# Kernel optimization log

Hardware: AMD Instinct MI355X
Metric: run time of the kernel (lower is better)

The kernel has to match this reference:

```python
import jax, jax.numpy as jnp
import numpy as np

B_, H_, W_, C_ = 4, 128, 128, 256
HEADS = 8
SPLIT = (8, 32)
POS_DIM = ((C_ // 2) // 4) // 4  # DynamicPosBias(dim//4).pos_dim with dim=C//2 -> 8


def _rel_tables(Hsp, Wsp):
    # rpe_biases: all relative (dy, dx) offsets, shape [(2Hsp-1)*(2Wsp-1), 2]
    gy, gx = np.meshgrid(np.arange(1 - Hsp, Hsp), np.arange(1 - Wsp, Wsp), indexing='ij')
    biases = np.stack([gy.ravel(), gx.ravel()], axis=1).astype(np.float32)
    # relative_position_index: [N, N] lookup into the bias table
    ch, cw = np.meshgrid(np.arange(Hsp), np.arange(Wsp), indexing='ij')
    cf = np.stack([ch.ravel(), cw.ravel()])  # [2, N]
    rel = (cf[:, :, None] - cf[:, None, :]).transpose(1, 2, 0)
    rel[..., 0] += Hsp - 1
    rel[..., 1] += Wsp - 1
    rel[..., 0] *= 2 * Wsp - 1
    idx = rel.sum(-1)
    return jnp.asarray(biases), jnp.asarray(idx)


def _ln(x, g, b):
    m = x.mean(-1, keepdims=True)
    v = ((x - m) ** 2).mean(-1, keepdims=True)
    return (x - m) / jnp.sqrt(v + 1e-5) * g + b


def _dyn_pos(biases, pw, pb, g1, b1, w1, c1, g2, b2, w2, c2, g3, b3, w3, c3):
    # DynamicPosBias, residual=False: pos3(pos2(pos1(pos_proj(b))))
    p = biases @ pw + pb
    p = jax.nn.relu(_ln(p, g1, b1)) @ w1 + c1
    p = jax.nn.relu(_ln(p, g2, b2)) @ w2 + c2
    p = jax.nn.relu(_ln(p, g3, b3)) @ w3 + c3
    return p  # [num_rel, heads]


def _win_attn(q, k, v, Hsp, Wsp, H, W, heads, pos_table, rel_idx):
    B, L, Cb = q.shape
    N = Hsp * Wsp
    hd = Cb // heads
    scale = hd ** (-0.5)

    def part(t):  # (B, L, Cb) -> (B*nW, heads, N, hd)
        t = t.reshape(B, H // Hsp, Hsp, W // Wsp, Wsp, Cb)
        t = t.transpose(0, 1, 3, 2, 4, 5).reshape(-1, N, heads, hd)
        return t.transpose(0, 2, 1, 3)

    qw, kw, vw = part(q) * scale, part(k), part(v)
    attn = jnp.einsum('whnd,whmd->whnm', qw, kw)
    rpb = pos_table[rel_idx.reshape(-1)].reshape(N, N, heads).transpose(2, 0, 1)
    attn = jax.nn.softmax(attn + rpb[None], axis=-1)
    ow = jnp.einsum('whnm,whmd->whnd', attn, vw)
    ow = ow.transpose(0, 2, 1, 3).reshape(-1, N, Cb)
    # windows2img
    img = ow.reshape(B, H // Hsp, W // Wsp, Hsp, Wsp, Cb)
    img = img.transpose(0, 1, 3, 2, 4, 5).reshape(B, H * W, Cb)
    return img


def setup_inputs() -> dict:
    key = jax.random.key(0)
    ks = jax.random.split(key, 16)
    nrm = lambda k, shp: jax.random.normal(k, shp, jnp.float32) * 0.02
    P, hb = POS_DIM, HEADS // 2
    d = {}
    d['x'] = jax.random.normal(ks[0], (B_, H_ * W_, C_), jnp.float32)
    d['w_qkv'] = nrm(ks[1], (C_, 3 * C_))
    d['w_proj'] = nrm(ks[2], (C_, C_))
    d['b_proj'] = jnp.zeros((C_,), jnp.float32)
    d['w_dw'] = nrm(ks[3], (C_, 1, 3, 3))
    d['b_dw'] = jnp.zeros((C_,), jnp.float32)
    d['pp_w'] = nrm(ks[4], (2, 2, P))
    d['pp_b'] = jnp.zeros((2, P), jnp.float32)
    d['ln1_g'] = jnp.ones((2, P), jnp.float32)
    d['ln1_b'] = jnp.zeros((2, P), jnp.float32)
    d['l1_w'] = nrm(ks[5], (2, P, P))
    d['l1_b'] = jnp.zeros((2, P), jnp.float32)
    d['ln2_g'] = jnp.ones((2, P), jnp.float32)
    d['ln2_b'] = jnp.zeros((2, P), jnp.float32)
    d['l2_w'] = nrm(ks[6], (2, P, P))
    d['l2_b'] = jnp.zeros((2, P), jnp.float32)
    d['ln3_g'] = jnp.ones((2, P), jnp.float32)
    d['ln3_b'] = jnp.zeros((2, P), jnp.float32)
    d['l3_w'] = nrm(ks[7], (2, P, hb))
    d['l3_b'] = jnp.zeros((2, hb), jnp.float32)
    d['H'] = H_
    d['W'] = W_
    return d


def reference(x, w_qkv, w_proj, b_proj, w_dw, b_dw, pp_w, pp_b, ln1_g, ln1_b, l1_w, l1_b, ln2_g, ln2_b, l2_w, l2_b, ln3_g, ln3_b, l3_w, l3_b, H, W):
    B, L, C = x.shape
    Cb, hb = C // 2, HEADS // 2
    qkv = (x @ w_qkv).reshape(B, L, 3, C).transpose(2, 0, 1, 3)
    q, k, v = qkv[0], qkv[1], qkv[2]
    v_img = v.transpose(0, 2, 1).reshape(B, C, H, W)
    outs = []
    for br in range(2):  # two cross-shaped window branches (idx=0/1)
        Hsp, Wsp = SPLIT if br == 0 else (SPLIT[1], SPLIT[0])
        sl = slice(br * Cb, (br + 1) * Cb)
        biases, rel_idx = _rel_tables(Hsp, Wsp)
        pos = _dyn_pos(biases, pp_w[br], pp_b[br], ln1_g[br], ln1_b[br], l1_w[br], l1_b[br],
                       ln2_g[br], ln2_b[br], l2_w[br], l2_b[br], ln3_g[br], ln3_b[br], l3_w[br], l3_b[br])
        outs.append(_win_attn(q[..., sl], k[..., sl], v[..., sl], Hsp, Wsp, H, W, hb, pos, rel_idx))
    att = jnp.concatenate(outs, axis=-1)  # (B, L, C)
    # LePE: depthwise 3x3 conv on V (get_v, groups=dim)
    lepe = jax.lax.conv_general_dilated(v_img, w_dw, (1, 1), ((1, 1), (1, 1)),
                                        feature_group_count=C,
                                        dimension_numbers=('NCHW', 'OIHW', 'NCHW'))
    lepe = (lepe + b_dw[None, :, None, None]).transpose(0, 2, 3, 1).reshape(B, L, C)
    return (att + lepe) @ w_proj + b_proj
```

## Files before the change

### kernel.cpp

```cpp
#include <hip/hip_runtime.h>
#include <hip/hip_bf16.h>
#include <math.h>

#define B_ 4
#define HH 128
#define WW 128
#define CC 256
#define LL (HH * WW)
#define NROWS (B_ * LL)
#define NREL 945
#define SCALE 0.17677669529663687f
#define LOG2E 1.4426950408889634f
#define SCALE2 (0.17677669529663687f * 1.4426950408889634f)

typedef __attribute__((ext_vector_type(8))) _Float16 half8;
typedef __attribute__((ext_vector_type(2))) __fp16 fp16x2;
typedef __attribute__((ext_vector_type(4))) float f32x4;

__device__ __forceinline__ unsigned short f2h(float f) {
    union { _Float16 h; unsigned short u; } v;
    v.h = (_Float16)f;
    return v.u;
}
__device__ __forceinline__ float h2f(unsigned short u) {
    union { unsigned short u; _Float16 h; } v;
    v.u = u;
    return (float)v.h;
}
__device__ __forceinline__ float exp2_raw(float x) {
    float r;
    asm("v_exp_f32 %0, %1" : "=v"(r) : "v"(x));
    return r;
}
__device__ __forceinline__ void gl_lds16(const unsigned short* g, unsigned short* l) {
    __builtin_amdgcn_global_load_lds((const __attribute__((address_space(1))) void*)g,
                                     (__attribute__((address_space(3))) void*)l, 16, 0, 0);
}

__device__ inline void ln_relu8(float* v, const float* g, const float* b) {
    float m = 0.f;
#pragma unroll
    for (int j = 0; j < 8; j++) m += v[j];
    m *= 0.125f;
    float var = 0.f;
#pragma unroll
    for (int j = 0; j < 8; j++) { float d = v[j] - m; var += d * d; }
    var *= 0.125f;
    float inv = 1.0f / sqrtf(var + 1e-5f);
#pragma unroll
    for (int j = 0; j < 8; j++) {
        float xn = (v[j] - m) * inv * g[j] + b[j];
        v[j] = xn > 0.f ? xn : 0.f;
    }
}

__device__ inline void mat8x8(const float* in, float* out, const float* w, const float* bias) {
#pragma unroll
    for (int j = 0; j < 8; j++) {
        float s = bias[j];
#pragma unroll
        for (int i = 0; i < 8; i++) s = fmaf(in[i], w[i * 8 + j], s);
        out[j] = s;
    }
}

__global__ void pos_kernel(const float* __restrict__ pp_w, const float* __restrict__ pp_b,
                           const float* __restrict__ ln1_g, const float* __restrict__ ln1_b,
                           const float* __restrict__ l1_w, const float* __restrict__ l1_b,
                           const float* __restrict__ ln2_g, const float* __restrict__ ln2_b,
                           const float* __restrict__ l2_w, const float* __restrict__ l2_b,
                           const float* __restrict__ ln3_g, const float* __restrict__ ln3_b,
                           const float* __restrict__ l3_w, const float* __restrict__ l3_b,
                           float* __restrict__ pos) {
    const int br = blockIdx.x;
    const int Wsp = br ? 8 : 32;
    const int Hsp = br ? 32 : 8;
    const int W2 = 2 * Wsp - 1;
    const int nrel = (2 * Hsp - 1) * W2;
    for (int r = threadIdx.x; r < nrel; r += blockDim.x) {
        float dy = (float)(r / W2 - (Hsp - 1));
        float dx = (float)(r % W2 - (Wsp - 1));
        float p[8], t[8];
#pragma unroll
        for (int j = 0; j < 8; j++)
            p[j] = dy * pp_w[br * 16 + j] + dx * pp_w[br * 16 + 8 + j] + pp_b[br * 8 + j];
        ln_relu8(p, ln1_g + br * 8, ln1_b + br * 8);
        mat8x8(p, t, l1_w + br * 64, l1_b + br * 8);
        ln_relu8(t, ln2_g + br * 8, ln2_b + br * 8);
        mat8x8(t, p, l2_w + br * 64, l2_b + br * 8);
        ln_relu8(p, ln3_g + br * 8, ln3_b + br * 8);
#pragma unroll
        for (int j = 0; j < 4; j++) {
            float s = l3_b[br * 4 + j];
#pragma unroll
            for (int i = 0; i < 8; i++) s = fmaf(p[i], l3_w[br * 32 + i * 4 + j], s);
            pos[(br * NREL + r) * 4 + j] = s;
        }
    }
}

__global__ void rpb_kernel(const float* __restrict__ pos, float* __restrict__ T2) {
    const int m = threadIdx.x;
    const int n = blockIdx.x;
    const int h = blockIdx.y;
    const int br = blockIdx.z;
    const int logW = br ? 3 : 5;
    const int Wsp = 1 << logW;
    const int Hsp = 256 >> logW;
    const int W2 = 2 * Wsp - 1;
    const int i_n = n >> logW, j_n = n & (Wsp - 1);
    const int i_m = m >> logW, j_m = m & (Wsp - 1);
    const int idx = (i_n - i_m + Hsp - 1) * W2 + (j_n - j_m + Wsp - 1);
    float v = pos[(br * NREL + idx) * 4 + h] * LOG2E;
    const int qs = n >> 4;
    const int ks = m >> 4;
    const int lane = ((n >> 2) & 3) * 16 + (m & 15);
    const int i = n & 3;
    T2[((((size_t)(br * 4 + h) * 16 + qs) * 16 + ks) * 64 + lane) * 4 + i] = v;
}

__global__ void convw_kernel(const float* __restrict__ w, unsigned short* __restrict__ th,
                             int Kd, int Nd) {
    int idx = blockIdx.x * blockDim.x + threadIdx.x;
    if (idx >= Kd * Nd) return;
    int n = idx / Kd, k = idx - n * Kd;
    th[idx] = f2h(w[(size_t)k * Nd + n]);
}

__global__ __launch_bounds__(256) void convx_kernel(const float* __restrict__ x,
                                                    unsigned short* __restrict__ xh) {
    size_t i = ((size_t)blockIdx.x * 256 + threadIdx.x) * 4;
    float4 v = *(const float4*)(x + i);
    ushort4 h;
    h.x = f2h(v.x); h.y = f2h(v.y); h.z = f2h(v.z); h.w = f2h(v.w);
    *(ushort4*)(xh + i) = h;
}

__global__ __launch_bounds__(256) void gemm_f16(const unsigned short* __restrict__ A,
                                                const unsigned short* __restrict__ B,
                                                unsigned short* __restrict__ C,
                                                int ldc, int nblk) {
    const int K = 256;
    __shared__ unsigned short sA[4096];
    __shared__ unsigned short sB[4096];

    const int tid = threadIdx.x;
    const int cpx = gridDim.x >> 3;
    const int bid = blockIdx.x;
    const int swz = (bid & 7) * cpx + (bid >> 3);
    const int nb = swz % nblk;
    const int mb = swz / nblk;
    const size_t blockM = (size_t)mb * 128;
    const int blockN = nb * 128;

    const int srow = tid >> 2;
    const int schunk = (tid & 3) * 8;
    const unsigned short* pA = A + (blockM + srow) * K + schunk;
    const unsigned short* pB = B + (size_t)(blockN + srow) * K + schunk;
    const size_t rstep = (size_t)64 * K;

    const int w = tid >> 6;
    const int lane = tid & 63;
    const int quad = lane >> 4;
    const int l15 = lane & 15;
    const int wm = (w & 1) * 64;
    const int wn = (w >> 1) * 64;

    f32x4 acc[4][4];
#pragma unroll
    for (int i = 0; i < 4; i++)
#pragma unroll
        for (int j = 0; j < 4; j++) acc[i][j] = (f32x4){0.f, 0.f, 0.f, 0.f};

    for (int kb = 0; kb < K; kb += 32) {
        gl_lds16(pA + kb, sA + tid * 8);
        gl_lds16(pA + kb + rstep, sA + 2048 + tid * 8);
        gl_lds16(pB + kb, sB + tid * 8);
        gl_lds16(pB + kb + rstep, sB + 2048 + tid * 8);
        __syncthreads();

        half8 fa[4], fb[4];
#pragma unroll
        for (int i = 0; i < 4; i++) {
            fa[i] = *(const half8*)(sA + (wm + i * 16 + l15) * 32 + quad * 8);
            fb[i] = *(const half8*)(sB + (wn + i * 16 + l15) * 32 + quad * 8);
        }
#pragma unroll
        for (int i = 0; i < 4; i++)
#pragma unroll
            for (int j = 0; j < 4; j++)
                acc[i][j] = __builtin_amdgcn_mfma_f32_16x16x32_f16(fa[i], fb[j], acc[i][j], 0, 0, 0);
        __syncthreads();
    }

#pragma unroll
    for (int j = 0; j < 4; j++) {
        int col = blockN + wn + j * 16 + l15;
        float sc = (ldc == 768 && col < 256) ? SCALE2 : 1.0f;
#pragma unroll
        for (int i = 0; i < 4; i++)
#pragma unroll
            for (int r = 0; r < 4; r++) {
                size_t row = blockM + wm + i * 16 + quad * 4 + r;
                C[row * ldc + col] = f2h(acc[i][j][r] * sc);
            }
    }
}

__global__ __launch_bounds__(256) void gemm_proj(const unsigned short* __restrict__ A,
                                                 const unsigned short* __restrict__ B,
                                                 float* __restrict__ C,
                                                 const float* __restrict__ bias) {
    const int K = 256;
    __shared__ unsigned short sA[4096];
    __shared__ unsigned short sB[4096];

    const int tid = threadIdx.x;
    const int cpx = gridDim.x >> 3;
    const int bid = blockIdx.x;
    const int swz = (bid & 7) * cpx + (bid >> 3);
    const int nb = swz & 1;
    const int mb = swz >> 1;
    const size_t blockM = (size_t)mb * 128;
    const int blockN = nb * 128;

    const int srow = tid >> 2;
    const int schunk = (tid & 3) * 8;
    const unsigned short* pA = A + (blockM + srow) * K + schunk;
    const unsigned short* pB = B + (size_t)(blockN + srow) * K + schunk;
    const size_t rstep = (size_t)64 * K;

    const int w = tid >> 6;
    const int lane = tid & 63;
    const int quad = lane >> 4;
    const int l15 = lane & 15;
    const int wm = (w & 1) * 64;
    const int wn = (w >> 1) * 64;

    f32x4 acc[4][4];
#pragma unroll
    for (int i = 0; i < 4; i++)
#pragma unroll
        for (int j = 0; j < 4; j++) acc[i][j] = (f32x4){0.f, 0.f, 0.f, 0.f};

    for (int kb = 0; kb < K; kb += 32) {
        gl_lds16(pA + kb, sA + tid * 8);
        gl_lds16(pA + kb + rstep, sA + 2048 + tid * 8);
        gl_lds16(pB + kb, sB + tid * 8);
        gl_lds16(pB + kb + rstep, sB + 2048 + tid * 8);
        __syncthreads();

        half8 fa[4], fb[4];
#pragma unroll
        for (int i = 0; i < 4; i++) {
            fa[i] = *(const half8*)(sA + (wm + i * 16 + l15) * 32 + quad * 8);
            fb[i] = *(const half8*)(sB + (wn + i * 16 + l15) * 32 + quad * 8);
        }
#pragma unroll
        for (int i = 0; i < 4; i++)
#pragma unroll
            for (int j = 0; j < 4; j++)
                acc[i][j] = __builtin_amdgcn_mfma_f32_16x16x32_f16(fa[i], fb[j], acc[i][j], 0, 0, 0);
        __syncthreads();
    }

#pragma unroll
    for (int j = 0; j < 4; j++) {
        int col = blockN + wn + j * 16 + l15;
        float bv = bias[col];
#pragma unroll
        for (int i = 0; i < 4; i++)
#pragma unroll
            for (int r = 0; r < 4; r++) {
                size_t row = blockM + wm + i * 16 + quad * 4 + r;
                C[row * 256 + col] = acc[i][j][r] + bv;
            }
    }
}

__global__ __launch_bounds__(256) void attn_mfma(const unsigned short* __restrict__ qkvb,
                                                 const float* __restrict__ T2,
                                                 unsigned short* __restrict__ attb) {
    __shared__ unsigned short Ks[256][32];
    __shared__ unsigned short Vt[32][264];
    __shared__ unsigned int   Pc[4][16][20];

    const int tid = threadIdx.x;
    const int wi = blockIdx.x;
    const int h = blockIdx.y;
    const int br = blockIdx.z;
    const int logW = br ? 3 : 5;
    const int Wsp = 1 << logW;
    const int Hsp = 256 >> logW;
    const int logNWx = br ? 4 : 2;
    const int b = wi >> 6;
    const int win = wi & 63;
    const int wy = win >> logNWx;
    const int wx = win & ((1 << logNWx) - 1);
    const int ccol = br * 128 + h * 32;

#pragma unroll
    for (int it = 0; it < 8; ++it) {
        int n = it * 32 + (tid >> 3);
        int d4 = (tid & 7) * 4;
        int iy = n >> logW, ix = n & (Wsp - 1);
        size_t row = ((size_t)b * LL + (wy * Hsp + iy) * WW + wx * Wsp + ix) * 768;
        ushort4 kv = *(const ushort4*)(qkvb + row + 256 + ccol + d4);
        ushort4 vv = *(const ushort4*)(qkvb + row + 512 + ccol + d4);
        *(ushort4*)&Ks[n][d4] = kv;
        int pos = (n & ~31) + 2 * (n & 15) + ((n >> 4) & 1);
        Vt[d4 + 0][pos] = vv.x;
        Vt[d4 + 1][pos] = vv.y;
        Vt[d4 + 2][pos] = vv.z;
        Vt[d4 + 3][pos] = vv.w;
    }
    __syncthreads();

    const int w = tid >> 6;
    const int lane = tid & 63;
    const int quad = lane >> 4;
    const int l15 = lane & 15;
    const f32x4 zero = {0.f, 0.f, 0.f, 0.f};

#pragma unroll 1
    for (int qt = 0; qt < 4; ++qt) {
        const int qbase = qt * 64 + w * 16;
        const int qrow = qbase + l15;
        const int iyq = qrow >> logW, ixq = qrow & (Wsp - 1);
        const size_t qpix = (size_t)b * LL + (wy * Hsp + iyq) * WW + wx * Wsp + ixq;
        half8 qfrag = *(const half8*)(qkvb + qpix * 768 + ccol + quad * 8);

        const float* Tf = T2 + (((size_t)(br * 4 + h) * 16 + (qt * 4 + w)) * 16) * 256 + lane * 4;

        f32x4 o0 = zero, o1 = zero;
        float rsum[4] = {0.f, 0.f, 0.f, 0.f};

#pragma unroll 2
        for (int kc = 0; kc < 8; ++kc) {
            const int kb0 = kc * 32;
            f32x4 b0 = *(const f32x4*)(Tf + (size_t)(kc * 2) * 256);
            f32x4 b1 = *(const f32x4*)(Tf + (size_t)(kc * 2 + 1) * 256);
            half8 kf0 = *(const half8*)&Ks[kb0 + l15][quad * 8];
            half8 kf1 = *(const half8*)&Ks[kb0 + 16 + l15][quad * 8];
            f32x4 s0 = __builtin_amdgcn_mfma_f32_16x16x32_f16(qfrag, kf0, b0, 0, 0, 0);
            f32x4 s1 = __builtin_amdgcn_mfma_f32_16x16x32_f16(qfrag, kf1, b1, 0, 0, 0);
#pragma unroll
            for (int i = 0; i < 4; ++i) {
                float e0 = exp2_raw(s0[i]);
                float e1 = exp2_raw(s1[i]);
                rsum[i] += e0 + e1;
                union { fp16x2 h; unsigned u; } cv;
                cv.h = __builtin_amdgcn_cvt_pkrtz(e0, e1);
                Pc[w][quad * 4 + i][l15] = cv.u;
            }
            half8 pf = *(const half8*)&Pc[w][l15][quad * 4];
            half8 vf0 = *(const half8*)&Vt[l15][kb0 + quad * 8];
            half8 vf1 = *(const half8*)&Vt[16 + l15][kb0 + quad * 8];
            o0 = __builtin_amdgcn_mfma_f32_16x16x32_f16(pf, vf0, o0, 0, 0, 0);
            o1 = __builtin_amdgcn_mfma_f32_16x16x32_f16(pf, vf1, o1, 0, 0, 0);
        }

#pragma unroll
        for (int i = 0; i < 4; ++i) {
            float s = rsum[i];
            s += __shfl_xor(s, 1, 64);
            s += __shfl_xor(s, 2, 64);
            s += __shfl_xor(s, 4, 64);
            s += __shfl_xor(s, 8, 64);
            rsum[i] = 1.0f / s;
        }

#pragma unroll
        for (int i = 0; i < 4; ++i) {
            int r = qbase + quad * 4 + i;
            int iyr = r >> logW, ixr = r & (Wsp - 1);
            size_t pix = (size_t)b * LL + (wy * Hsp + iyr) * WW + wx * Wsp + ixr;
            unsigned short* op = attb + pix * 256 + ccol;
            op[l15] = f2h(o0[i] * rsum[i]);
            op[16 + l15] = f2h(o1[i] * rsum[i]);
        }
    }
}

__global__ __launch_bounds__(256) void lepe_kernel(const unsigned short* __restrict__ qkvb,
                                                   const float* __restrict__ w_dw,
                                                   const float* __restrict__ b_dw,
                                                   unsigned short* __restrict__ attb) {
    const int tid = threadIdx.x;
    const int c4 = (tid & 63) * 4;
    const int pix = blockIdx.x * 4 + (tid >> 6);
    const int bb = pix >> 14;
    const int y = (pix >> 7) & 127;
    const int x = pix & 127;

    float wreg[36];
    const float* wp = w_dw + c4 * 9;
#pragma unroll
    for (int q = 0; q < 9; q++) {
        float4 t = *(const float4*)(wp + q * 4);
        wreg[q * 4 + 0] = t.x; wreg[q * 4 + 1] = t.y;
        wreg[q * 4 + 2] = t.z; wreg[q * 4 + 3] = t.w;
    }

    float4 bv = *(const float4*)(b_dw + c4);
    ushort4 av = *(const ushort4*)(attb + ((size_t)pix << 8) + c4);
    float4 acc;
    acc.x = h2f(av.x) + bv.x; acc.y = h2f(av.y) + bv.y;
    acc.z = h2f(av.z) + bv.z; acc.w = h2f(av.w) + bv.w;

#pragma unroll
    for (int ky = 0; ky < 3; ky++) {
        int yy = y + ky - 1;
        if (yy < 0 || yy > 127) continue;
#pragma unroll
        for (int kx = 0; kx < 3; kx++) {
            int xx = x + kx - 1;
            if (xx < 0 || xx > 127) continue;
            int j = ky * 3 + kx;
            ushort4 v = *(const ushort4*)(qkvb + (((size_t)bb << 14) + yy * 128 + xx) * 768 + 512 + c4);
            acc.x = fmaf(h2f(v.x), wreg[0 * 9 + j], acc.x);
            acc.y = fmaf(h2f(v.y), wreg[1 * 9 + j], acc.y);
            acc.z = fmaf(h2f(v.z), wreg[2 * 9 + j], acc.z);
            acc.w = fmaf(h2f(v.w), wreg[3 * 9 + j], acc.w);
        }
    }
    ushort4 r;
    r.x = f2h(acc.x); r.y = f2h(acc.y); r.z = f2h(acc.z); r.w = f2h(acc.w);
    *(ushort4*)(attb + ((size_t)pix << 8) + c4) = r;
}

extern "C" void kernel_launch(void* const* d_in, const int* in_sizes, int n_in,
                              void* d_out, int out_size, void* d_ws, size_t ws_size,
                              hipStream_t stream) {
    const float* x     = (const float*)d_in[0];
    const float* w_qkv = (const float*)d_in[1];
    const float* w_proj= (const float*)d_in[2];
    const float* b_proj= (const float*)d_in[3];
    const float* w_dw  = (const float*)d_in[4];
    const float* b_dw  = (const float*)d_in[5];
    const float* pp_w  = (const float*)d_in[6];
    const float* pp_b  = (const float*)d_in[7];
    const float* ln1_g = (const float*)d_in[8];
    const float* ln1_b = (const float*)d_in[9];
    const float* l1_w  = (const float*)d_in[10];
    const float* l1_b  = (const float*)d_in[11];
    const float* ln2_g = (const float*)d_in[12];
    const float* ln2_b = (const float*)d_in[13];
    const float* l2_w  = (const float*)d_in[14];
    const float* l2_b  = (const float*)d_in[15];
    const float* ln3_g = (const float*)d_in[16];
    const float* ln3_b = (const float*)d_in[17];
    const float* l3_w  = (const float*)d_in[18];
    const float* l3_b  = (const float*)d_in[19];

    float* pos = (float*)d_ws;
    float* T2  = pos + 7680;
    unsigned short* qkvb = (unsigned short*)(T2 + 524288);
    unsigned short* attb = qkvb + (size_t)NROWS * 768;
    unsigned short* xh   = attb + (size_t)NROWS * 256;
    unsigned short* wqh  = xh + (size_t)NROWS * 256;
    unsigned short* wph  = wqh + 768 * 256;

    pos_kernel<<<2, 128, 0, stream>>>(pp_w, pp_b, ln1_g, ln1_b, l1_w, l1_b,
                                      ln2_g, ln2_b, l2_w, l2_b, ln3_g, ln3_b,
                                      l3_w, l3_b, pos);
    rpb_kernel<<<dim3(256, 4, 2), 256, 0, stream>>>(pos, T2);
    convw_kernel<<<768, 256, 0, stream>>>(w_qkv, wqh, 256, 768);
    convw_kernel<<<256, 256, 0, stream>>>(w_proj, wph, 256, 256);
    convx_kernel<<<NROWS / 4, 256, 0, stream>>>(x, xh);
    gemm_f16<<<(NROWS / 128) * 6, 256, 0, stream>>>(xh, wqh, qkvb, 768, 6);
    attn_mfma<<<dim3(256, 4, 2), 256, 0, stream>>>(qkvb, T2, attb);
    lepe_kernel<<<(B_ * LL) / 4, 256, 0, stream>>>(qkvb, w_dw, b_dw, attb);
    gemm_proj<<<(NROWS / 128) * 2, 256, 0, stream>>>(attb, wph, (float*)d_out, b_proj);
}
```

Measured before the change: 352.7 us.

## Use sliding-window row reuse in LePE depthwise conv, one wave per 16-row column strip

The LePE depthwise 3x3 kernel now assigns each wave a vertical strip of 16 pixels in one column and keeps three rows of V taps in registers, loading only one new row per output pixel. This cuts redundant V reads from nine per pixel to about three. The grid drops to 1024 blocks, which lowers parallelism and adds register pressure, and each thread now runs a serial loop.

Result: faster. 327.2 us (-7.2%).

```diff
diff --git a/kernel.cpp b/kernel.cpp
--- a/kernel.cpp
+++ b/kernel.cpp
@@ -386,12 +386,14 @@
                                                    const float* __restrict__ w_dw,
                                                    const float* __restrict__ b_dw,
                                                    unsigned short* __restrict__ attb) {
-    const int tid = threadIdx.x;
-    const int c4 = (tid & 63) * 4;
-    const int pix = blockIdx.x * 4 + (tid >> 6);
-    const int bb = pix >> 14;
-    const int y = (pix >> 7) & 127;
-    const int x = pix & 127;
+    const int lane = threadIdx.x & 63;
+    const int wv = threadIdx.x >> 6;
+    const int c4 = lane * 4;
+    const int gid = blockIdx.x * 4 + wv;
+    const int ys = gid & 7;
+    const int x  = (gid >> 3) & 127;
+    const int b  = gid >> 10;
+    const int y0 = ys * 16;
 
     float wreg[36];
     const float* wp = w_dw + c4 * 9;
@@ -401,32 +403,57 @@
         wreg[q * 4 + 0] = t.x; wreg[q * 4 + 1] = t.y;
         wreg[q * 4 + 2] = t.z; wreg[q * 4 + 3] = t.w;
     }
-
-    float4 bv = *(const float4*)(b_dw + c4);
-    ushort4 av = *(const ushort4*)(attb + ((size_t)pix << 8) + c4);
-    float4 acc;
-    acc.x = h2f(av.x) + bv.x; acc.y = h2f(av.y) + bv.y;
-    acc.z = h2f(av.z) + bv.z; acc.w = h2f(av.w) + bv.w;
-
-#pragma unroll
-    for (int ky = 0; ky < 3; ky++) {
-        int yy = y + ky - 1;
-        if (yy < 0 || yy > 127) continue;
-#pragma unroll
-        for (int kx = 0; kx < 3; kx++) {
-            int xx = x + kx - 1;
-            if (xx < 0 || xx > 127) continue;
-            int j = ky * 3 + kx;
-            ushort4 v = *(const ushort4*)(qkvb + (((size_t)bb << 14) + yy * 128 + xx) * 768 + 512 + c4);
-            acc.x = fmaf(h2f(v.x), wreg[0 * 9 + j], acc.x);
-            acc.y = fmaf(h2f(v.y), wreg[1 * 9 + j], acc.y);
-            acc.z = fmaf(h2f(v.z), wreg[2 * 9 + j], acc.z);
-            acc.w = fmaf(h2f(v.w), wreg[3 * 9 + j], acc.w);
-        }
-    }
-    ushort4 r;
-    r.x = f2h(acc.x); r.y = f2h(acc.y); r.z = f2h(acc.z); r.w = f2h(acc.w);
-    *(ushort4*)(attb + ((size_t)pix << 8) + c4) = r;
+    const float4 bv = *(const float4*)(b_dw + c4);
+    const float4 z4 = {0.f, 0.f, 0.f, 0.f};
+    const bool xm_ok = (x > 0), xp_ok = (x < 127);
+
+    const unsigned short* vp = qkvb + (((size_t)b << 14) + x) * 768 + 512 + c4;
+
+    float4 r0[3], r1[3], r2[3];
+
+#define LDV(yy, dx, dst) { \
+        ushort4 u = *(const ushort4*)(vp + (ptrdiff_t)(yy) * 98304 + (dx) * 768); \
+        dst.x = h2f(u.x); dst.y = h2f(u.y); dst.z = h2f(u.z); dst.w = h2f(u.w); }
+#define LDROW(yy, d) { \
+        if ((yy) < 0 || (yy) > 127) { d[0] = z4; d[1] = z4; d[2] = z4; } \
+        else { \
+            if (xm_ok) LDV(yy, -1, d[0]) else d[0] = z4; \
+            LDV(yy, 0, d[1]); \
+            if (xp_ok) LDV(yy, 1, d[2]) else d[2] = z4; } }
+#define TAP(rv, j) \
+        acc.x = fmaf(rv.x, wreg[0 * 9 + (j)], acc.x); \
+        acc.y = fmaf(rv.y, wreg[1 * 9 + (j)], acc.y); \
+        acc.z = fmaf(rv.z, wreg[2 * 9 + (j)], acc.z); \
+        acc.w = fmaf(rv.w, wreg[3 * 9 + (j)], acc.w);
+
+    LDROW(y0 - 1, r0)
+    LDROW(y0, r1)
+
+#pragma unroll
+    for (int t = 0; t < 16; ++t) {
+        const int y = y0 + t;
+        LDROW(y + 1, r2)
+
+        const size_t opx = ((((size_t)b << 14) + y * 128 + x) << 8) + c4;
+        ushort4 av = *(const ushort4*)(attb + opx);
+        float4 acc;
+        acc.x = h2f(av.x) + bv.x; acc.y = h2f(av.y) + bv.y;
+        acc.z = h2f(av.z) + bv.z; acc.w = h2f(av.w) + bv.w;
+
+        TAP(r0[0], 0) TAP(r0[1], 1) TAP(r0[2], 2)
+        TAP(r1[0], 3) TAP(r1[1], 4) TAP(r1[2], 5)
+        TAP(r2[0], 6) TAP(r2[1], 7) TAP(r2[2], 8)
+
+        ushort4 o;
+        o.x = f2h(acc.x); o.y = f2h(acc.y); o.z = f2h(acc.z); o.w = f2h(acc.w);
+        *(ushort4*)(attb + opx) = o;
+
+        r0[0] = r1[0]; r0[1] = r1[1]; r0[2] = r1[2];
+        r1[0] = r2[0]; r1[1] = r2[1]; r1[2] = r2[2];
+    }
+#undef LDV
+#undef LDROW
+#undef TAP
 }
 
 extern "C" void kernel_launch(void* const* d_in, const int* in_sizes, int n_in,
@@ -470,6 +497,6 @@
     convx_kernel<<<NROWS / 4, 256, 0, stream>>>(x, xh);
     gemm_f16<<<(NROWS / 128) * 6, 256, 0, stream>>>(xh, wqh, qkvb, 768, 6);
     attn_mfma<<<dim3(256, 4, 2), 256, 0, stream>>>(qkvb, T2, attb);
-    lepe_kernel<<<(B_ * LL) / 4, 256, 0, stream>>>(qkvb, w_dw, b_dw, attb);
+    lepe_kernel<<<1024, 256, 0, stream>>>(qkvb, w_dw, b_dw, attb);
     gemm_proj<<<(NROWS / 128) * 2, 256, 0, stream>>>(attb, wph, (float*)d_out, b_proj);
 }
```
